# Performance work log

Measured on AMD Instinct MI355X. Metric: run time of the kernel, lower is better.

## Reference

```python
import jax, jax.numpy as jnp
import numpy as np

MAX_LENGTH = 10
SOS = 0
H = 1024
V = 32000
B = 256
S = 64


def setup_inputs() -> dict:
    key = jax.random.key(0)
    ks = jax.random.split(key, 16)
    sc = 1.0 / np.sqrt(H)
    return {
        "encoder_outputs": jax.random.normal(ks[0], (B, S, H), jnp.float32),
        "encoder_hidden": jax.random.normal(ks[1], (1, B, H), jnp.float32),
        "target_tensor": jax.random.randint(ks[2], (B, MAX_LENGTH), 0, V),
        "embedding": jax.random.normal(ks[3], (V, H), jnp.float32),
        "Wa_w": jax.random.uniform(ks[4], (H, H), jnp.float32, -sc, sc),
        "Wa_b": jax.random.uniform(ks[5], (H,), jnp.float32, -sc, sc),
        "Ua_w": jax.random.uniform(ks[6], (H, H), jnp.float32, -sc, sc),
        "Ua_b": jax.random.uniform(ks[7], (H,), jnp.float32, -sc, sc),
        "Va_w": jax.random.uniform(ks[8], (1, H), jnp.float32, -sc, sc),
        "Va_b": jax.random.uniform(ks[9], (1,), jnp.float32, -sc, sc),
        "gru_w_ih": jax.random.uniform(ks[10], (3 * H, 2 * H), jnp.float32, -sc, sc),
        "gru_w_hh": jax.random.uniform(ks[11], (3 * H, H), jnp.float32, -sc, sc),
        "gru_b_ih": jax.random.uniform(ks[12], (3 * H,), jnp.float32, -sc, sc),
        "gru_b_hh": jax.random.uniform(ks[13], (3 * H,), jnp.float32, -sc, sc),
        "out_w": jax.random.uniform(ks[14], (V, H), jnp.float32, -sc, sc),
        "out_b": jax.random.uniform(ks[15], (V,), jnp.float32, -sc, sc),
    }


def reference(encoder_outputs, encoder_hidden, target_tensor, embedding,
              Wa_w, Wa_b, Ua_w, Ua_b, Va_w, Va_b,
              gru_w_ih, gru_w_hh, gru_b_ih, gru_b_hh, out_w, out_b):
    keys = encoder_outputs                      # [B,S,H]
    # Ua(keys) is step-invariant: hoist out of the decode loop.
    Uk = jnp.einsum('bsh,kh->bsk', keys, Ua_w) + Ua_b  # [B,S,H]
    h0 = encoder_hidden[0]                      # [B,H]
    # teacher forcing: input at step i is SOS for i=0 else target[:, i-1]
    toks = jnp.concatenate(
        [jnp.full((B, 1), SOS, dtype=target_tensor.dtype),
         target_tensor[:, :MAX_LENGTH - 1]], axis=1).T  # [T,B]

    def step(h, tok):
        emb = embedding[tok]                               # [B,H] (dropout = identity in eval)
        wq = jnp.dot(h, Wa_w.T) + Wa_b                     # [B,H]
        e = jnp.tanh(wq[:, None, :] + Uk)                  # [B,S,H]
        scores = jnp.einsum('bsh,h->bs', e, Va_w[0]) + Va_b[0]
        w = jax.nn.softmax(scores, axis=-1)                # [B,S]
        ctx = jnp.einsum('bs,bsh->bh', w, keys)            # [B,H]
        x = jnp.concatenate([emb, ctx], axis=-1)           # [B,2H]
        gi = jnp.dot(x, gru_w_ih.T) + gru_b_ih             # [B,3H]
        gh = jnp.dot(h, gru_w_hh.T) + gru_b_hh             # [B,3H]
        ir, iz, inn = jnp.split(gi, 3, axis=-1)
        hr, hz, hn = jnp.split(gh, 3, axis=-1)
        r = jax.nn.sigmoid(ir + hr)
        z = jax.nn.sigmoid(iz + hz)
        n = jnp.tanh(inn + r * hn)
        h2 = (1.0 - z) * n + z * h                         # [B,H]
        logits = jnp.dot(h2, out_w.T) + out_b              # [B,V]
        return h2, (logits, w)

    h_last, (logits, attn) = jax.lax.scan(step, h0, toks)
    dec_out = jax.nn.log_softmax(jnp.transpose(logits, (1, 0, 2)), axis=-1)  # [B,T,V]
    attentions = jnp.transpose(attn, (1, 0, 2))            # [B,T,S]
    return dec_out, h_last[None, :, :], attentions
```

## Files before the change

### kernel.cpp

```cpp
#include <hip/hip_runtime.h>
#include <math.h>

#define H 1024
#define V 32000
#define B 256
#define S 64
#define T 10

#define GBK 32

typedef __attribute__((ext_vector_type(8))) short bf16x8;
typedef __attribute__((ext_vector_type(4))) float f32x4;

static __device__ __forceinline__ unsigned short f2bf(float f) {
  unsigned int u = __float_as_uint(f);
  u += 0x7fff + ((u >> 16) & 1);
  return (unsigned short)(u >> 16);
}
static __device__ __forceinline__ float bf2f(unsigned short u) {
  return __uint_as_float(((unsigned int)u) << 16);
}
static __device__ __forceinline__ float fast_tanh(float x) {
  float e = __expf(2.f * x);
  return 1.f - 2.f * __builtin_amdgcn_rcpf(e + 1.f);
}
static __device__ __forceinline__ float fast_sigmoid(float x) {
  return __builtin_amdgcn_rcpf(1.f + __expf(-x));
}

static __device__ __forceinline__ void load_lds16(const void* g, void* l) {
  __builtin_amdgcn_global_load_lds(
      (const __attribute__((address_space(1))) unsigned int*)g,
      (__attribute__((address_space(3))) unsigned int*)l, 16, 0, 0);
}

static __device__ __forceinline__ int lds_off(int row, int g) {
  return row * GBK + ((g ^ ((row >> 1) & 3)) * 8);
}

template <int TM, int TN, int MODE, int GRIDMODE, int STAGES>
__global__ __launch_bounds__(256) void gemm_mfma(
    const unsigned short* __restrict__ A, const unsigned short* __restrict__ W,
    const float* __restrict__ aux, float* __restrict__ C,
    unsigned short* __restrict__ Cb, float* __restrict__ partials,
    int M, int N, int K, int ldc, int pstride) {
  constexpr int FM = (TM == 128) ? 4 : 2;
  constexpr int FN = (TN == 128) ? 4 : 2;
  constexpr int CA = TM / 64;
  constexpr int CB = TN / 64;
  constexpr int LOADS = CA + CB;

  __shared__ unsigned short lsA[STAGES][TM * GBK];
  __shared__ unsigned short lsB[STAGES][TN * GBK];
  const int tid = threadIdx.x;
  const int lane = tid & 63;
  const int w = tid >> 6;

  int mIdx, nIdx;
  if constexpr (GRIDMODE == 1) {
    const int nwg = gridDim.x * gridDim.y;
    const int orig = blockIdx.y * gridDim.x + blockIdx.x;
    const int q = nwg >> 3, rr = nwg & 7;
    const int xcd = orig & 7, rest = orig >> 3;
    const int wgid =
        (xcd < rr ? xcd * (q + 1) : rr * (q + 1) + (xcd - rr) * q) + rest;
    mIdx = wgid % gridDim.x;
    nIdx = wgid / gridDim.x;
  } else {
    mIdx = blockIdx.y;
    nIdx = blockIdx.x;
  }
  const int mBase = mIdx * TM;
  const int nBase = nIdx * TN;
  const int rowBase = (w >> 1) * (TM / 2);
  const int colBase = (w & 1) * (TN / 2);

  const int fr = lane & 15;
  const int fkU = lane >> 4;
  const int fg = lane >> 4;

  f32x4 acc[FM][FN] = {};

  auto STAGE = [&](int buf, int k0) {
#pragma unroll
    for (int i = 0; i < CA; ++i) {
      int chunk = i * 256 + tid;
      int row = chunk >> 2;
      int u = chunk & 3;
      int col = (u ^ ((row >> 1) & 3)) * 8;
      load_lds16(A + (size_t)(mBase + row) * K + k0 + col,
                 &lsA[buf][chunk * 8]);
    }
#pragma unroll
    for (int i = 0; i < CB; ++i) {
      int chunk = i * 256 + tid;
      int row = chunk >> 2;
      int u = chunk & 3;
      int col = (u ^ ((row >> 1) & 3)) * 8;
      load_lds16(W + (size_t)(nBase + row) * K + k0 + col,
                 &lsB[buf][chunk * 8]);
    }
  };

  const int NT = K / GBK;
  STAGE(0, 0);
  if constexpr (STAGES == 3) STAGE(1, GBK);
  int cb = 0;
  for (int t = 0; t < NT; ++t) {
    if constexpr (STAGES == 3) {
      if (t + 1 < NT) {
        asm volatile("s_waitcnt vmcnt(%0)\n\ts_barrier" :: "i"(LOADS)
                     : "memory");
      } else {
        asm volatile("s_waitcnt vmcnt(0)\n\ts_barrier" ::: "memory");
      }
      if (t + 2 < NT) STAGE((cb + 2) % 3, (t + 2) * GBK);
    } else {
      asm volatile("s_waitcnt vmcnt(0)\n\ts_barrier" ::: "memory");
      if (t + 1 < NT) STAGE(cb ^ 1, (t + 1) * GBK);
    }

    bf16x8 af[FM], bfr[FN];
#pragma unroll
    for (int m = 0; m < FM; ++m)
      af[m] = *(const bf16x8*)&lsA[cb][lds_off(rowBase + m * 16 + fr, fkU)];
#pragma unroll
    for (int n = 0; n < FN; ++n)
      bfr[n] = *(const bf16x8*)&lsB[cb][lds_off(colBase + n * 16 + fr, fkU)];
#pragma unroll
    for (int m = 0; m < FM; ++m)
#pragma unroll
      for (int n = 0; n < FN; ++n)
        acc[m][n] = __builtin_amdgcn_mfma_f32_16x16x32_bf16(
            af[m], bfr[n], acc[m][n], 0, 0, 0);
    cb = (STAGES == 3) ? (cb + 1) % 3 : (cb ^ 1);
  }

#pragma unroll
  for (int m = 0; m < FM; ++m) {
    int colg[FN];
    float bv[FN];
#pragma unroll
    for (int n = 0; n < FN; ++n) {
      colg[n] = nBase + colBase + n * 16 + fr;
      if constexpr (MODE != 2) bv[n] = aux[colg[n]];
    }
#pragma unroll
    for (int r = 0; r < 4; ++r) {
      const int rowg = mBase + rowBase + m * 16 + fg * 4 + r;
      float v[FN];
#pragma unroll
      for (int n = 0; n < FN; ++n) {
        if constexpr (MODE == 2)
          v[n] = acc[m][n][r] + aux[(size_t)rowg * ldc + colg[n]];
        else
          v[n] = acc[m][n][r] + bv[n];
        if constexpr (MODE == 1 || MODE == 3)
          Cb[(size_t)rowg * ldc + colg[n]] = f2bf(v[n]);
        else
          C[(size_t)rowg * ldc + colg[n]] = v[n];
      }
      if constexpr (MODE == 3) {
        float mx = fmaxf(fmaxf(v[0], v[1]), fmaxf(v[2], v[3]));
        mx = fmaxf(mx, __shfl_xor(mx, 1, 64));
        mx = fmaxf(mx, __shfl_xor(mx, 2, 64));
        mx = fmaxf(mx, __shfl_xor(mx, 4, 64));
        mx = fmaxf(mx, __shfl_xor(mx, 8, 64));
        float se = __expf(v[0] - mx) + __expf(v[1] - mx) +
                   __expf(v[2] - mx) + __expf(v[3] - mx);
        se += __shfl_xor(se, 1, 64);
        se += __shfl_xor(se, 2, 64);
        se += __shfl_xor(se, 4, 64);
        se += __shfl_xor(se, 8, 64);
        if (fr == 0) {
          float2* pp = (float2*)partials;
          pp[(size_t)rowg * pstride + nIdx * 2 + (w & 1)] =
              make_float2(mx, se);
        }
      }
    }
  }
}

__global__ __launch_bounds__(256) void cvt_bf16_kernel(
    const float* __restrict__ src, unsigned short* __restrict__ dst) {
  size_t i = ((size_t)blockIdx.x * 256 + threadIdx.x) * 8;
  float4 a = *(const float4*)&src[i];
  float4 b = *(const float4*)&src[i + 4];
  ushort4 lo, hi;
  lo.x = f2bf(a.x); lo.y = f2bf(a.y); lo.z = f2bf(a.z); lo.w = f2bf(a.w);
  hi.x = f2bf(b.x); hi.y = f2bf(b.y); hi.z = f2bf(b.z); hi.w = f2bf(b.w);
  *(ushort4*)&dst[i] = lo;
  *(ushort4*)&dst[i + 4] = hi;
}

__global__ __launch_bounds__(256) void cvt_split_wih(
    const float* __restrict__ w_ih, unsigned short* __restrict__ Wemb,
    unsigned short* __restrict__ Wctx) {
  size_t base = ((size_t)blockIdx.x * 256 + threadIdx.x) * 8;
  int row = (int)(base >> 11);
  int col = (int)(base & 2047);
  float4 a = *(const float4*)&w_ih[base];
  float4 b = *(const float4*)&w_ih[base + 4];
  ushort4 lo, hi;
  lo.x = f2bf(a.x); lo.y = f2bf(a.y); lo.z = f2bf(a.z); lo.w = f2bf(a.w);
  hi.x = f2bf(b.x); hi.y = f2bf(b.y); hi.z = f2bf(b.z); hi.w = f2bf(b.w);
  unsigned short* dst = (col < H) ? (Wemb + (size_t)row * H + col)
                                  : (Wctx + (size_t)row * H + col - H);
  *(ushort4*)dst = lo;
  *(ushort4*)(dst + 4) = hi;
}

__global__ __launch_bounds__(256) void build_fused_bias(
    const float* __restrict__ Wa_b, const float* __restrict__ b_hh,
    float* __restrict__ fb) {
  int i = blockIdx.x * 256 + threadIdx.x;
  fb[i] = (i < H) ? Wa_b[i] : b_hh[i - H];
}

__global__ __launch_bounds__(256) void embed_all_kernel(
    const int* __restrict__ target, const float* __restrict__ emb,
    unsigned short* __restrict__ embAll) {
  int idx = blockIdx.x * 256 + threadIdx.x;
  int h8 = (idx & 127) * 8;
  int tb = idx >> 7;
  int t = tb >> 8;
  int b = tb & 255;
  int tok = (t == 0) ? 0 : target[b * T + (t - 1)];
  const float* e = emb + (size_t)tok * H + h8;
  float4 a = *(const float4*)e;
  float4 c = *(const float4*)(e + 4);
  ushort4 lo, hi;
  lo.x = f2bf(a.x); lo.y = f2bf(a.y); lo.z = f2bf(a.z); lo.w = f2bf(a.w);
  hi.x = f2bf(c.x); hi.y = f2bf(c.y); hi.z = f2bf(c.z); hi.w = f2bf(c.w);
  unsigned short* d = embAll + (size_t)tb * H + h8;
  *(ushort4*)d = lo;
  *(ushort4*)(d + 4) = hi;
}

__global__ __launch_bounds__(256) void attn_fused_kernel(
    const float* __restrict__ wqgh, const unsigned short* __restrict__ Uk_bf,
    const unsigned short* __restrict__ keys_bf,
    const float* __restrict__ Va_w, const float* __restrict__ Va_b,
    float* __restrict__ out_attn, unsigned short* __restrict__ ctx_bf, int t) {
  const int b = blockIdx.x;
  const int tid = threadIdx.x;
  __shared__ float wqs[H];
  __shared__ float vas[H];
  __shared__ float sw[S];

  ((float4*)wqs)[tid] = ((const float4*)(wqgh + (size_t)b * 4 * H))[tid];
  ((float4*)vas)[tid] = ((const float4*)Va_w)[tid];
  __syncthreads();

  const int s = tid >> 2;
  const int hc = (tid & 3) * 256;
  const unsigned short* uk = Uk_bf + ((size_t)b * S + s) * H + hc;
  float sum = 0.f;
#pragma unroll 4
  for (int i = 0; i < 256; i += 8) {
    bf16x8 u = *(const bf16x8*)&uk[i];
#pragma unroll
    for (int j = 0; j < 8; ++j) {
      float e = fast_tanh(wqs[hc + i + j] + bf2f((unsigned short)u[j]));
      sum += e * vas[hc + i + j];
    }
  }
  sum += __shfl_xor(sum, 1, 64);
  sum += __shfl_xor(sum, 2, 64);
  if ((tid & 3) == 0) sw[s] = sum + Va_b[0];
  __syncthreads();

  if (tid < 64) {
    float v = sw[tid];
    float m = v;
    for (int off = 32; off > 0; off >>= 1) m = fmaxf(m, __shfl_xor(m, off, 64));
    float e = __expf(v - m);
    float sm = e;
    for (int off = 32; off > 0; off >>= 1) sm += __shfl_xor(sm, off, 64);
    float wv = e / sm;
    sw[tid] = wv;
    out_attn[((size_t)b * T + t) * S + tid] = wv;
  }
  __syncthreads();

  const unsigned short* kb = keys_bf + (size_t)b * S * H + tid * 4;
  float c0 = 0.f, c1 = 0.f, c2 = 0.f, c3 = 0.f;
#pragma unroll 8
  for (int s2 = 0; s2 < S; ++s2) {
    float wv = sw[s2];
    ushort4 kv = *(const ushort4*)&kb[(size_t)s2 * H];
    c0 += wv * bf2f(kv.x);
    c1 += wv * bf2f(kv.y);
    c2 += wv * bf2f(kv.z);
    c3 += wv * bf2f(kv.w);
  }
  ushort4 o;
  o.x = f2bf(c0); o.y = f2bf(c1); o.z = f2bf(c2); o.w = f2bf(c3);
  *(ushort4*)&ctx_bf[(size_t)b * H + tid * 4] = o;
}

__global__ __launch_bounds__(256) void gru_kernel(
    const float* __restrict__ gi, const float* __restrict__ wqgh,
    const float* __restrict__ h_in, float* __restrict__ h_out,
    unsigned short* __restrict__ h_out_bf) {
  int idx = blockIdx.x * 256 + threadIdx.x;
  int b = idx >> 10;
  int j = idx & (H - 1);
  const float* gib = gi + (size_t)b * 3 * H;
  const float* ghb = wqgh + (size_t)b * 4 * H + H;
  float r = fast_sigmoid(gib[j] + ghb[j]);
  float z = fast_sigmoid(gib[H + j] + ghb[H + j]);
  float n = fast_tanh(gib[2 * H + j] + r * ghb[2 * H + j]);
  float hp = h_in[idx];
  float ho = (1.f - z) * n + z * hp;
  h_out[idx] = ho;
  h_out_bf[idx] = f2bf(ho);
}

__global__ __launch_bounds__(256) void logsm_reduce_kernel(
    const float* __restrict__ partials, float* __restrict__ ls, int P) {
  const int row = blockIdx.x;
  const int tid = threadIdx.x;
  const float2* pp = (const float2*)partials + (size_t)row * P;
  __shared__ float red[256];
  float mx = -INFINITY;
  for (int i = tid; i < P; i += 256) mx = fmaxf(mx, pp[i].x);
  red[tid] = mx;
  __syncthreads();
  for (int off = 128; off > 0; off >>= 1) {
    if (tid < off) red[tid] = fmaxf(red[tid], red[tid + off]);
    __syncthreads();
  }
  mx = red[0];
  __syncthreads();
  float sm = 0.f;
  for (int i = tid; i < P; i += 256) sm += pp[i].y * __expf(pp[i].x - mx);
  red[tid] = sm;
  __syncthreads();
  for (int off = 128; off > 0; off >>= 1) {
    if (tid < off) red[tid] += red[tid + off];
    __syncthreads();
  }
  if (tid == 0) ls[row] = mx + __logf(red[0]);
}

__global__ __launch_bounds__(256) void logsm_sub_kernel(
    const unsigned short* __restrict__ logits_bf, const float* __restrict__ ls,
    float* __restrict__ dec) {
  const int tb = blockIdx.y;
  const int t = tb >> 8;
  const int b = tb & 255;
  const int i8 = (blockIdx.x * 256 + threadIdx.x) * 8;
  if (i8 < V) {
    float l = ls[tb];
    const unsigned short* src = logits_bf + (size_t)tb * V + i8;
    bf16x8 u = *(const bf16x8*)src;
    float* d = dec + (size_t)b * T * V + (size_t)t * V + i8;
    float4 o0, o1;
    o0.x = bf2f((unsigned short)u[0]) - l; o0.y = bf2f((unsigned short)u[1]) - l;
    o0.z = bf2f((unsigned short)u[2]) - l; o0.w = bf2f((unsigned short)u[3]) - l;
    o1.x = bf2f((unsigned short)u[4]) - l; o1.y = bf2f((unsigned short)u[5]) - l;
    o1.z = bf2f((unsigned short)u[6]) - l; o1.w = bf2f((unsigned short)u[7]) - l;
    *(float4*)d = o0;
    *(float4*)(d + 4) = o1;
  }
}

__global__ __launch_bounds__(256) void copy_kernel(
    const float* __restrict__ src, float* __restrict__ dst, int n) {
  int i = blockIdx.x * 256 + threadIdx.x;
  if (i < n) dst[i] = src[i];
}

extern "C" void kernel_launch(void* const* d_in, const int* in_sizes, int n_in,
                              void* d_out, int out_size, void* d_ws, size_t ws_size,
                              hipStream_t stream) {
  const float* keys       = (const float*)d_in[0];
  const float* enc_hidden = (const float*)d_in[1];
  const int*   target     = (const int*)d_in[2];
  const float* embedding  = (const float*)d_in[3];
  const float* Wa_w = (const float*)d_in[4];
  const float* Wa_b = (const float*)d_in[5];
  const float* Ua_w = (const float*)d_in[6];
  const float* Ua_b = (const float*)d_in[7];
  const float* Va_w = (const float*)d_in[8];
  const float* Va_b = (const float*)d_in[9];
  const float* gru_w_ih = (const float*)d_in[10];
  const float* gru_w_hh = (const float*)d_in[11];
  const float* gru_b_ih = (const float*)d_in[12];
  const float* gru_b_hh = (const float*)d_in[13];
  const float* out_w = (const float*)d_in[14];
  const float* out_b = (const float*)d_in[15];

  float* out = (float*)d_out;
  float* out_dec  = out;
  float* out_h    = out + (size_t)B * T * V;
  float* out_attn = out + (size_t)B * T * V + (size_t)B * H;

  char* p = (char*)d_ws;
  unsigned short* keys_bf = (unsigned short*)p; p += (size_t)B * S * H * 2;
  unsigned short* outw_bf = (unsigned short*)p; p += (size_t)V * H * 2;
  unsigned short* Uaw_bf  = (unsigned short*)p; p += (size_t)H * H * 2;
  unsigned short* fusedW  = (unsigned short*)p; p += (size_t)4 * H * H * 2;
  float*          fusedB  = (float*)p;          p += (size_t)4 * H * 4;
  unsigned short* Wemb_bf = (unsigned short*)p; p += (size_t)3 * H * H * 2;
  unsigned short* Wctx_bf = (unsigned short*)p; p += (size_t)3 * H * H * 2;
  unsigned short* embAll  = (unsigned short*)p; p += (size_t)T * B * H * 2;
  unsigned short* Uk_bf   = (unsigned short*)p; p += (size_t)B * S * H * 2;
  float*          giE     = (float*)p;          p += (size_t)T * B * 3 * H * 4;
  float*          wqgh    = (float*)p;          p += (size_t)B * 4 * H * 4;
  unsigned short* ctx_bf  = (unsigned short*)p; p += (size_t)B * H * 2;
  float*          gi      = (float*)p;          p += (size_t)B * 3 * H * 4;
  float*          hA      = (float*)p;          p += (size_t)B * H * 4;
  float*          hB      = (float*)p;          p += (size_t)B * H * 4;
  unsigned short* hAll    = (unsigned short*)p; p += (size_t)(T + 1) * B * H * 2;
  unsigned short* logits_bf = (unsigned short*)p; p += (size_t)T * B * V * 2;
  float*          parts   = (float*)p;          p += (size_t)T * B * 500 * 2 * 4;
  float*          ls      = (float*)p;          p += (size_t)T * B * 4;

  cvt_bf16_kernel<<<(B * S * H) / 2048, 256, 0, stream>>>(keys, keys_bf);
  cvt_bf16_kernel<<<((size_t)V * H) / 2048, 256, 0, stream>>>(out_w, outw_bf);
  cvt_bf16_kernel<<<(H * H) / 2048, 256, 0, stream>>>(Ua_w, Uaw_bf);
  cvt_bf16_kernel<<<(H * H) / 2048, 256, 0, stream>>>(Wa_w, fusedW);
  cvt_bf16_kernel<<<(3 * H * H) / 2048, 256, 0, stream>>>(gru_w_hh,
                                                          fusedW + (size_t)H * H);
  build_fused_bias<<<(4 * H) / 256, 256, 0, stream>>>(Wa_b, gru_b_hh, fusedB);
  cvt_split_wih<<<(3 * H * 2 * H) / 2048, 256, 0, stream>>>(gru_w_ih, Wemb_bf,
                                                            Wctx_bf);
  embed_all_kernel<<<(T * B * H / 8) / 256, 256, 0, stream>>>(target, embedding,
                                                              embAll);
  cvt_bf16_kernel<<<(B * H) / 2048, 256, 0, stream>>>(enc_hidden, hAll);

  gemm_mfma<128, 128, 1, 0, 2>
      <<<dim3(H / 128, (B * S) / 128), 256, 0, stream>>>(
          keys_bf, Uaw_bf, Ua_b, nullptr, Uk_bf, nullptr, B * S, H, H, H, 0);
  gemm_mfma<128, 128, 0, 1, 2>
      <<<dim3((T * B) / 128, 3 * H / 128), 256, 0, stream>>>(
          embAll, Wemb_bf, gru_b_ih, giE, nullptr, nullptr, T * B, 3 * H, H,
          3 * H, 0);

  const float* h_in = enc_hidden;
  float* hbufs[2] = {hA, hB};

  for (int t = 0; t < T; ++t) {
    const unsigned short* hbf_in = hAll + (size_t)t * B * H;
    unsigned short* hbf_out = hAll + (size_t)(t + 1) * B * H;
    float* h_out = hbufs[t & 1];

    gemm_mfma<64, 64, 0, 1, 3><<<dim3(B / 64, 4 * H / 64), 256, 0, stream>>>(
        hbf_in, fusedW, fusedB, wqgh, nullptr, nullptr, B, 4 * H, H, 4 * H, 0);
    attn_fused_kernel<<<B, 256, 0, stream>>>(
        wqgh, Uk_bf, keys_bf, Va_w, Va_b, out_attn, ctx_bf, t);
    gemm_mfma<64, 64, 2, 1, 3><<<dim3(B / 64, 3 * H / 64), 256, 0, stream>>>(
        ctx_bf, Wctx_bf, giE + (size_t)t * B * 3 * H, gi, nullptr, nullptr,
        B, 3 * H, H, 3 * H, 0);
    gru_kernel<<<(B * H) / 256, 256, 0, stream>>>(gi, wqgh, h_in, h_out,
                                                  hbf_out);

    h_in = h_out;
  }

  gemm_mfma<128, 128, 3, 1, 2>
      <<<dim3((T * B) / 128, V / 128), 256, 0, stream>>>(
          hAll + (size_t)B * H, outw_bf, out_b, nullptr, logits_bf, parts,
          T * B, V, H, V, 500);
  logsm_reduce_kernel<<<T * B, 256, 0, stream>>>(parts, ls, 500);
  logsm_sub_kernel<<<dim3((V + 2047) / 2048, T * B), 256, 0, stream>>>(
      logits_bf, ls, out_dec);

  copy_kernel<<<(B * H + 255) / 256, 256, 0, stream>>>(h_in, out_h, B * H);
}
```

Baseline: 1.026 ms.

## Fuse decode loop into one persistent kernel with grid-wide barriers

Replaces the 40 per-step launches (two GEMMs, attention, GRU) with a single persistent kernel of 256 workgroups. Phases are separated by a software grid barrier built on atomics, and the final hidden-state copy is folded into the last step. This removes launch overhead and kernel-boundary drain across the serial decode loop. The cost is barrier latency, and correctness depends on all 256 workgroups being resident at once. The per-step GEMMs now use a fixed 64x64 tile per workgroup, with some workgroups idle during the 3H GEMM.

```diff
diff --git a/kernel.cpp b/kernel.cpp
--- a/kernel.cpp
+++ b/kernel.cpp
@@ -8,6 +8,7 @@
 #define T 10
 
 #define GBK 32
+#define NWG 256
 
 typedef __attribute__((ext_vector_type(8))) short bf16x8;
 typedef __attribute__((ext_vector_type(4))) float f32x4;
@@ -36,6 +37,242 @@
 
 static __device__ __forceinline__ int lds_off(int row, int g) {
   return row * GBK + ((g ^ ((row >> 1) & 3)) * 8);
+}
+
+static __device__ __forceinline__ void gbar(unsigned* cnt, unsigned* gen) {
+  __syncthreads();
+  if (threadIdx.x == 0) {
+    __threadfence();
+    unsigned g =
+        __hip_atomic_load(gen, __ATOMIC_ACQUIRE, __HIP_MEMORY_SCOPE_AGENT);
+    unsigned a = __hip_atomic_fetch_add(cnt, 1u, __ATOMIC_ACQ_REL,
+                                        __HIP_MEMORY_SCOPE_AGENT);
+    if (a == NWG - 1) {
+      __hip_atomic_store(cnt, 0u, __ATOMIC_RELAXED, __HIP_MEMORY_SCOPE_AGENT);
+      __hip_atomic_fetch_add(gen, 1u, __ATOMIC_ACQ_REL,
+                             __HIP_MEMORY_SCOPE_AGENT);
+    } else {
+      while (__hip_atomic_load(gen, __ATOMIC_ACQUIRE,
+                               __HIP_MEMORY_SCOPE_AGENT) == g)
+        __builtin_amdgcn_s_sleep(8);
+    }
+    __threadfence();
+  }
+  __syncthreads();
+}
+
+template <int MODE>
+static __device__ void gemm64_dev(
+    const unsigned short* __restrict__ A, const unsigned short* __restrict__ W,
+    const float* __restrict__ aux, float* __restrict__ C, int ldc,
+    int mBase, int nBase,
+    unsigned short (&lsA)[3][64 * GBK], unsigned short (&lsB)[3][64 * GBK]) {
+  const int tid = threadIdx.x;
+  const int lane = tid & 63;
+  const int w = tid >> 6;
+  const int rowBase = (w >> 1) * 32;
+  const int colBase = (w & 1) * 32;
+  const int fr = lane & 15;
+  const int fkU = lane >> 4;
+  const int fg = lane >> 4;
+
+  f32x4 acc[2][2] = {};
+
+  auto STAGE = [&](int buf, int k0) {
+    int row = tid >> 2;
+    int u = tid & 3;
+    int col = (u ^ ((row >> 1) & 3)) * 8;
+    load_lds16(A + (size_t)(mBase + row) * H + k0 + col, &lsA[buf][tid * 8]);
+    load_lds16(W + (size_t)(nBase + row) * H + k0 + col, &lsB[buf][tid * 8]);
+  };
+
+  asm volatile("s_waitcnt vmcnt(0)" ::: "memory");
+  const int NT = H / GBK;
+  STAGE(0, 0);
+  STAGE(1, GBK);
+  int cb = 0;
+  for (int t = 0; t < NT; ++t) {
+    if (t + 1 < NT) {
+      asm volatile("s_waitcnt vmcnt(2)\n\ts_barrier" ::: "memory");
+    } else {
+      asm volatile("s_waitcnt vmcnt(0)\n\ts_barrier" ::: "memory");
+    }
+    if (t + 2 < NT) STAGE((cb + 2) % 3, (t + 2) * GBK);
+
+    bf16x8 af[2], bfr[2];
+#pragma unroll
+    for (int m = 0; m < 2; ++m)
+      af[m] = *(const bf16x8*)&lsA[cb][lds_off(rowBase + m * 16 + fr, fkU)];
+#pragma unroll
+    for (int n = 0; n < 2; ++n)
+      bfr[n] = *(const bf16x8*)&lsB[cb][lds_off(colBase + n * 16 + fr, fkU)];
+#pragma unroll
+    for (int m = 0; m < 2; ++m)
+#pragma unroll
+      for (int n = 0; n < 2; ++n)
+        acc[m][n] = __builtin_amdgcn_mfma_f32_16x16x32_bf16(
+            af[m], bfr[n], acc[m][n], 0, 0, 0);
+    cb = (cb + 1) % 3;
+  }
+
+#pragma unroll
+  for (int m = 0; m < 2; ++m)
+#pragma unroll
+    for (int n = 0; n < 2; ++n) {
+      const int colg = nBase + colBase + n * 16 + fr;
+#pragma unroll
+      for (int r = 0; r < 4; ++r) {
+        const int rowg = mBase + rowBase + m * 16 + fg * 4 + r;
+        float v;
+        if constexpr (MODE == 2)
+          v = acc[m][n][r] + aux[(size_t)rowg * ldc + colg];
+        else
+          v = acc[m][n][r] + aux[colg];
+        C[(size_t)rowg * ldc + colg] = v;
+      }
+    }
+}
+
+__global__ __launch_bounds__(256) void decoder_loop_kernel(
+    unsigned short* __restrict__ hAll,
+    const unsigned short* __restrict__ fusedW,
+    const float* __restrict__ fusedB,
+    const unsigned short* __restrict__ Uk_bf,
+    const unsigned short* __restrict__ keys_bf,
+    const float* __restrict__ Va_w, const float* __restrict__ Va_b,
+    const unsigned short* __restrict__ Wctx_bf,
+    const float* __restrict__ giE,
+    const float* __restrict__ enc_hidden,
+    float* __restrict__ hA, float* __restrict__ hB,
+    float* __restrict__ wqgh,
+    unsigned short* __restrict__ ctx_bf,
+    float* __restrict__ gi,
+    float* __restrict__ out_attn,
+    float* __restrict__ out_h,
+    unsigned* __restrict__ bar) {
+  __shared__ unsigned short lsA[3][64 * GBK];
+  __shared__ unsigned short lsB[3][64 * GBK];
+  __shared__ float wqs[H];
+  __shared__ float vas[H];
+  __shared__ float sw[S];
+
+  const int g = blockIdx.x;
+  const int tid = threadIdx.x;
+  unsigned* cnt = bar;
+  unsigned* gen = bar + 1;
+
+  for (int t = 0; t < T; ++t) {
+    const unsigned short* hbf_in = hAll + (size_t)t * B * H;
+    unsigned short* hbf_out = hAll + (size_t)(t + 1) * B * H;
+    const float* h_in = (t == 0) ? enc_hidden : ((t & 1) ? hA : hB);
+    float* h_out = (t & 1) ? hB : hA;
+
+    gemm64_dev<0>(hbf_in, fusedW, fusedB, wqgh, 4 * H, (g & 3) * 64,
+                  (g >> 2) * 64, lsA, lsB);
+    gbar(cnt, gen);
+
+    {
+      const int b = g;
+      ((float4*)wqs)[tid] = ((const float4*)(wqgh + (size_t)b * 4 * H))[tid];
+      ((float4*)vas)[tid] = ((const float4*)Va_w)[tid];
+      __syncthreads();
+
+      const int s = tid >> 2;
+      const int hc = (tid & 3) * 256;
+      const unsigned short* uk = Uk_bf + ((size_t)b * S + s) * H + hc;
+      float sum = 0.f;
+#pragma unroll 4
+      for (int i = 0; i < 256; i += 8) {
+        bf16x8 u = *(const bf16x8*)&uk[i];
+#pragma unroll
+        for (int j = 0; j < 8; ++j) {
+          float e = fast_tanh(wqs[hc + i + j] + bf2f((unsigned short)u[j]));
+          sum += e * vas[hc + i + j];
+        }
+      }
+      sum += __shfl_xor(sum, 1, 64);
+      sum += __shfl_xor(sum, 2, 64);
+      if ((tid & 3) == 0) sw[s] = sum + Va_b[0];
+      __syncthreads();
+
+      if (tid < 64) {
+        float v = sw[tid];
+        float m = v;
+        for (int off = 32; off > 0; off >>= 1)
+          m = fmaxf(m, __shfl_xor(m, off, 64));
+        float e = __expf(v - m);
+        float sm = e;
+        for (int off = 32; off > 0; off >>= 1) sm += __shfl_xor(sm, off, 64);
+        float wv = e / sm;
+        sw[tid] = wv;
+        out_attn[((size_t)b * T + t) * S + tid] = wv;
+      }
+      __syncthreads();
+
+      const unsigned short* kb = keys_bf + (size_t)b * S * H + tid * 4;
+      float c0 = 0.f, c1 = 0.f, c2 = 0.f, c3 = 0.f;
+#pragma unroll 8
+      for (int s2 = 0; s2 < S; ++s2) {
+        float wv = sw[s2];
+        ushort4 kv = *(const ushort4*)&kb[(size_t)s2 * H];
+        c0 += wv * bf2f(kv.x);
+        c1 += wv * bf2f(kv.y);
+        c2 += wv * bf2f(kv.z);
+        c3 += wv * bf2f(kv.w);
+      }
+      ushort4 o;
+      o.x = f2bf(c0); o.y = f2bf(c1); o.z = f2bf(c2); o.w = f2bf(c3);
+      *(ushort4*)&ctx_bf[(size_t)b * H + tid * 4] = o;
+    }
+    gbar(cnt, gen);
+
+    if (g < 192) {
+      gemm64_dev<2>(ctx_bf, Wctx_bf, giE + (size_t)t * B * 3 * H, gi, 3 * H,
+                    (g & 3) * 64, (g >> 2) * 64, lsA, lsB);
+    }
+    gbar(cnt, gen);
+
+    {
+      const int idx = (g * 256 + tid) * 4;
+      const int b = idx >> 10;
+      const int j = idx & (H - 1);
+      const float* gib = gi + (size_t)b * 3 * H;
+      const float* ghb = wqgh + (size_t)b * 4 * H + H;
+      float4 gr4 = *(const float4*)&gib[j];
+      float4 gz4 = *(const float4*)&gib[H + j];
+      float4 gn4 = *(const float4*)&gib[2 * H + j];
+      float4 hr4 = *(const float4*)&ghb[j];
+      float4 hz4 = *(const float4*)&ghb[H + j];
+      float4 hn4 = *(const float4*)&ghb[2 * H + j];
+      float4 hp4 = *(const float4*)&h_in[idx];
+      float4 ho4;
+      ushort4 hb4;
+      {
+        float r0 = fast_sigmoid(gr4.x + hr4.x);
+        float z0 = fast_sigmoid(gz4.x + hz4.x);
+        float n0 = fast_tanh(gn4.x + r0 * hn4.x);
+        ho4.x = (1.f - z0) * n0 + z0 * hp4.x;
+        float r1 = fast_sigmoid(gr4.y + hr4.y);
+        float z1 = fast_sigmoid(gz4.y + hz4.y);
+        float n1 = fast_tanh(gn4.y + r1 * hn4.y);
+        ho4.y = (1.f - z1) * n1 + z1 * hp4.y;
+        float r2 = fast_sigmoid(gr4.z + hr4.z);
+        float z2 = fast_sigmoid(gz4.z + hz4.z);
+        float n2 = fast_tanh(gn4.z + r2 * hn4.z);
+        ho4.z = (1.f - z2) * n2 + z2 * hp4.z;
+        float r3 = fast_sigmoid(gr4.w + hr4.w);
+        float z3 = fast_sigmoid(gz4.w + hz4.w);
+        float n3 = fast_tanh(gn4.w + r3 * hn4.w);
+        ho4.w = (1.f - z3) * n3 + z3 * hp4.w;
+      }
+      hb4.x = f2bf(ho4.x); hb4.y = f2bf(ho4.y);
+      hb4.z = f2bf(ho4.z); hb4.w = f2bf(ho4.w);
+      *(float4*)&h_out[idx] = ho4;
+      *(ushort4*)&hbf_out[idx] = hb4;
+      if (t == T - 1) *(float4*)&out_h[idx] = ho4;
+    }
+    gbar(cnt, gen);
+  }
 }
 
 template <int TM, int TN, int MODE, int GRIDMODE, int STAGES>
@@ -236,86 +473,6 @@
   unsigned short* d = embAll + (size_t)tb * H + h8;
   *(ushort4*)d = lo;
   *(ushort4*)(d + 4) = hi;
-}
-
-__global__ __launch_bounds__(256) void attn_fused_kernel(
-    const float* __restrict__ wqgh, const unsigned short* __restrict__ Uk_bf,
-    const unsigned short* __restrict__ keys_bf,
-    const float* __restrict__ Va_w, const float* __restrict__ Va_b,
-    float* __restrict__ out_attn, unsigned short* __restrict__ ctx_bf, int t) {
-  const int b = blockIdx.x;
-  const int tid = threadIdx.x;
-  __shared__ float wqs[H];
-  __shared__ float vas[H];
-  __shared__ float sw[S];
-
-  ((float4*)wqs)[tid] = ((const float4*)(wqgh + (size_t)b * 4 * H))[tid];
-  ((float4*)vas)[tid] = ((const float4*)Va_w)[tid];
-  __syncthreads();
-
-  const int s = tid >> 2;
-  const int hc = (tid & 3) * 256;
-  const unsigned short* uk = Uk_bf + ((size_t)b * S + s) * H + hc;
-  float sum = 0.f;
-#pragma unroll 4
-  for (int i = 0; i < 256; i += 8) {
-    bf16x8 u = *(const bf16x8*)&uk[i];
-#pragma unroll
-    for (int j = 0; j < 8; ++j) {
-      float e = fast_tanh(wqs[hc + i + j] + bf2f((unsigned short)u[j]));
-      sum += e * vas[hc + i + j];
-    }
-  }
-  sum += __shfl_xor(sum, 1, 64);
-  sum += __shfl_xor(sum, 2, 64);
-  if ((tid & 3) == 0) sw[s] = sum + Va_b[0];
-  __syncthreads();
-
-  if (tid < 64) {
-    float v = sw[tid];
-    float m = v;
-    for (int off = 32; off > 0; off >>= 1) m = fmaxf(m, __shfl_xor(m, off, 64));
-    float e = __expf(v - m);
-    float sm = e;
-    for (int off = 32; off > 0; off >>= 1) sm += __shfl_xor(sm, off, 64);
-    float wv = e / sm;
-    sw[tid] = wv;
-    out_attn[((size_t)b * T + t) * S + tid] = wv;
-  }
-  __syncthreads();
-
-  const unsigned short* kb = keys_bf + (size_t)b * S * H + tid * 4;
-  float c0 = 0.f, c1 = 0.f, c2 = 0.f, c3 = 0.f;
-#pragma unroll 8
-  for (int s2 = 0; s2 < S; ++s2) {
-    float wv = sw[s2];
-    ushort4 kv = *(const ushort4*)&kb[(size_t)s2 * H];
-    c0 += wv * bf2f(kv.x);
-    c1 += wv * bf2f(kv.y);
-    c2 += wv * bf2f(kv.z);
-    c3 += wv * bf2f(kv.w);
-  }
-  ushort4 o;
-  o.x = f2bf(c0); o.y = f2bf(c1); o.z = f2bf(c2); o.w = f2bf(c3);
-  *(ushort4*)&ctx_bf[(size_t)b * H + tid * 4] = o;
-}
-
-__global__ __launch_bounds__(256) void gru_kernel(
-    const float* __restrict__ gi, const float* __restrict__ wqgh,
-    const float* __restrict__ h_in, float* __restrict__ h_out,
-    unsigned short* __restrict__ h_out_bf) {
-  int idx = blockIdx.x * 256 + threadIdx.x;
-  int b = idx >> 10;
-  int j = idx & (H - 1);
-  const float* gib = gi + (size_t)b * 3 * H;
-  const float* ghb = wqgh + (size_t)b * 4 * H + H;
-  float r = fast_sigmoid(gib[j] + ghb[j]);
-  float z = fast_sigmoid(gib[H + j] + ghb[H + j]);
-  float n = fast_tanh(gib[2 * H + j] + r * ghb[2 * H + j]);
-  float hp = h_in[idx];
-  float ho = (1.f - z) * n + z * hp;
-  h_out[idx] = ho;
-  h_out_bf[idx] = f2bf(ho);
 }
 
 __global__ __launch_bounds__(256) void logsm_reduce_kernel(
@@ -365,12 +522,6 @@
     *(float4*)d = o0;
     *(float4*)(d + 4) = o1;
   }
-}
-
-__global__ __launch_bounds__(256) void copy_kernel(
-    const float* __restrict__ src, float* __restrict__ dst, int n) {
-  int i = blockIdx.x * 256 + threadIdx.x;
-  if (i < n) dst[i] = src[i];
 }
 
 extern "C" void kernel_launch(void* const* d_in, const int* in_sizes, int n_in,
@@ -418,6 +569,9 @@
   unsigned short* logits_bf = (unsigned short*)p; p += (size_t)T * B * V * 2;
   float*          parts   = (float*)p;          p += (size_t)T * B * 500 * 2 * 4;
   float*          ls      = (float*)p;          p += (size_t)T * B * 4;
+  unsigned*       barrier = (unsigned*)p;       p += 256;
+
+  hipMemsetAsync(barrier, 0, 256, stream);
 
   cvt_bf16_kernel<<<(B * S * H) / 2048, 256, 0, stream>>>(keys, keys_bf);
   cvt_bf16_kernel<<<((size_t)V * H) / 2048, 256, 0, stream>>>(out_w, outw_bf);
@@ -440,26 +594,9 @@
           embAll, Wemb_bf, gru_b_ih, giE, nullptr, nullptr, T * B, 3 * H, H,
           3 * H, 0);
 
-  const float* h_in = enc_hidden;
-  float* hbufs[2] = {hA, hB};
-
-  for (int t = 0; t < T; ++t) {
-    const unsigned short* hbf_in = hAll + (size_t)t * B * H;
-    unsigned short* hbf_out = hAll + (size_t)(t + 1) * B * H;
-    float* h_out = hbufs[t & 1];
-
-    gemm_mfma<64, 64, 0, 1, 3><<<dim3(B / 64, 4 * H / 64), 256, 0, stream>>>(
-        hbf_in, fusedW, fusedB, wqgh, nullptr, nullptr, B, 4 * H, H, 4 * H, 0);
-    attn_fused_kernel<<<B, 256, 0, stream>>>(
-        wqgh, Uk_bf, keys_bf, Va_w, Va_b, out_attn, ctx_bf, t);
-    gemm_mfma<64, 64, 2, 1, 3><<<dim3(B / 64, 3 * H / 64), 256, 0, stream>>>(
-        ctx_bf, Wctx_bf, giE + (size_t)t * B * 3 * H, gi, nullptr, nullptr,
-        B, 3 * H, H, 3 * H, 0);
-    gru_kernel<<<(B * H) / 256, 256, 0, stream>>>(gi, wqgh, h_in, h_out,
-                                                  hbf_out);
-
-    h_in = h_out;
-  }
+  decoder_loop_kernel<<<NWG, 256, 0, stream>>>(
+      hAll, fusedW, fusedB, Uk_bf, keys_bf, Va_w, Va_b, Wctx_bf, giE,
+      enc_hidden, hA, hB, wqgh, ctx_bf, gi, out_attn, out_h, barrier);
 
   gemm_mfma<128, 128, 3, 1, 2>
       <<<dim3((T * B) / 128, V / 128), 256, 0, stream>>>(
@@ -468,6 +605,4 @@
   logsm_reduce_kernel<<<T * B, 256, 0, stream>>>(parts, ls, 500);
   logsm_sub_kernel<<<dim3((V + 2047) / 2048, T * B), 256, 0, stream>>>(
       logits_bf, ls, out_dec);
-
-  copy_kernel<<<(B * H + 255) / 256, 256, 0, stream>>>(h_in, out_h, B * H);
-}
+}
```

Measured after the change: 2.771 ms. 2.7x slower.
